# Kernel tuning notes

Hardware: AMD Instinct MI355X
Metric: run time of the kernel (lower is better)

## Reference

```python
import math
import jax, jax.numpy as jnp
from jax import lax
import numpy as np

B, S2, D = 8, 1024, 768  # seq_len = 32*32 spatial tokens
HD = 64                   # head_dim
K = 7                     # LocalRmsNorm kernel_size
EPS = 1e-7


def setup_inputs() -> dict:
    key = jax.random.key(0)
    ks = jax.random.split(key, 6)
    sc = 0.02
    return {
        "x": jax.random.normal(ks[0], (B, S2, D), jnp.float32),
        "norm_w": jnp.ones((D,), jnp.float32),
        "wq": jax.random.normal(ks[1], (D, D), jnp.float32) * sc,
        "bq": jnp.zeros((D,), jnp.float32),
        "wk": jax.random.normal(ks[2], (D, D), jnp.float32) * sc,
        "bk": jnp.zeros((D,), jnp.float32),
        "wv": jax.random.normal(ks[3], (D, D), jnp.float32) * sc,
        "bv": jnp.zeros((D,), jnp.float32),
        "wo": jax.random.normal(ks[4], (D, D), jnp.float32) * sc,
        "bo": jnp.zeros((D,), jnp.float32),
    }


def local_rms_norm(x, w):
    # x: [b, s*s, d]; sliding KxK box-sum of squares over the s x s grid,
    # zero-padded (matches F.unfold), mean divisor is always K*K.
    b, ss, d = x.shape
    s = int(math.isqrt(ss))
    sq = (x * x).reshape(b, s, s, d)
    box = lax.reduce_window(sq, 0.0, lax.add,
                            (1, K, K, 1), (1, 1, 1, 1), 'SAME')
    rms = jnp.sqrt(EPS + box / (K * K)).reshape(b, ss, d)
    return x / rms * w


def reference(x, norm_w, wq, bq, wk, bk, wv, bv, wo, bo):
    xn = local_rms_norm(x, norm_w)
    b, s, d = xn.shape
    h = d // HD

    def proj(w_, b_):
        return (xn @ w_.T + b_).reshape(b, s, h, HD).transpose(0, 2, 1, 3)

    q = proj(wq, bq)  # [b, h, s, dh]
    k = proj(wk, bk)
    v = proj(wv, bv)
    scores = jnp.einsum('bhqd,bhkd->bhqk', q, k) / math.sqrt(HD)
    attn = jax.nn.softmax(scores, axis=-1)
    out = jnp.einsum('bhqk,bhkd->bhqd', attn, v)
    out = out.transpose(0, 2, 1, 3).reshape(b, s, d)
    return out @ wo.T + bo
```

## Files before the change

### kernel.cpp

```cpp
#include <hip/hip_runtime.h>

typedef _Float16 f16x8 __attribute__((ext_vector_type(8)));
typedef _Float16 f16x4 __attribute__((ext_vector_type(4)));
typedef _Float16 f16x2 __attribute__((ext_vector_type(2)));
typedef float    f32x4 __attribute__((ext_vector_type(4)));
typedef float    f32x16 __attribute__((ext_vector_type(16)));
typedef unsigned int u32x4 __attribute__((ext_vector_type(4)));
typedef unsigned short ushort_t;
typedef unsigned int uint_t;

#define LOG2E 1.44269504088896340736f

__device__ __forceinline__ ushort_t f2h(float x) {
  _Float16 h = (_Float16)x;
  return __builtin_bit_cast(ushort_t, h);
}

__device__ __forceinline__ uint_t packpair(float a, float b) {
  return __builtin_bit_cast(uint_t, __builtin_amdgcn_cvt_pkrtz(a, b));
}

__device__ __forceinline__ f16x8 mk8(uint_t a, uint_t b, uint_t c, uint_t d) {
  u32x4 t; t[0] = a; t[1] = b; t[2] = c; t[3] = d;
  return __builtin_bit_cast(f16x8, t);
}

__device__ __forceinline__ void gload_lds16(const void* g, void* lds) {
  __builtin_amdgcn_global_load_lds(
      (const __attribute__((address_space(1))) void*)(uintptr_t)g,
      (__attribute__((address_space(3))) void*)(unsigned)(uintptr_t)lds,
      16, 0, 0);
}


__global__ __launch_bounds__(256)
void lrn_a(const float* __restrict__ x, ushort_t* __restrict__ tmp) {
  int tid = blockIdx.x * 256 + threadIdx.x;
  int dv  = tid % 192;
  int rem = tid / 192;
  int pos = rem & 1023;
  int b   = rem >> 10;
  int r = pos >> 5, c = pos & 31;
  const float4* base = (const float4*)x + ((size_t)b * 1024 + (size_t)r * 32) * 192 + dv;
  float ax = 0.f, ay = 0.f, az = 0.f, aw = 0.f;
#pragma unroll
  for (int dc = -3; dc <= 3; ++dc) {
    int cc = c + dc;
    if (cc >= 0 && cc < 32) {
      float4 v = base[cc * 192];
      ax += v.x * v.x; ay += v.y * v.y; az += v.z * v.z; aw += v.w * v.w;
    }
  }
  f16x4 o;
  o[0] = (_Float16)ax; o[1] = (_Float16)ay; o[2] = (_Float16)az; o[3] = (_Float16)aw;
  *(f16x4*)(tmp + (size_t)tid * 4) = o;
}

__global__ __launch_bounds__(256)
void lrn_b(const float* __restrict__ x, const ushort_t* __restrict__ tmp,
           const float* __restrict__ wn, ushort_t* __restrict__ xn) {
  int tid = blockIdx.x * 256 + threadIdx.x;
  int dv  = tid % 192;
  int rem = tid / 192;
  int pos = rem & 1023;
  int b   = rem >> 10;
  int r = pos >> 5, c = pos & 31;
  const ushort_t* tb = tmp + (((size_t)b * 1024 + c) * 192 + dv) * 4;
  float ax = 0.f, ay = 0.f, az = 0.f, aw = 0.f;
#pragma unroll
  for (int dr = -3; dr <= 3; ++dr) {
    int rr = r + dr;
    if (rr >= 0 && rr < 32) {
      f16x4 v = *(const f16x4*)(tb + (size_t)rr * 24576);
      ax += (float)v[0]; ay += (float)v[1]; az += (float)v[2]; aw += (float)v[3];
    }
  }
  float4 xv = ((const float4*)x)[tid];
  float4 wv = ((const float4*)wn)[dv];
  const float inv49 = 1.0f / 49.0f;
  float i0 = 1.0f / sqrtf(1e-7f + ax * inv49);
  float i1 = 1.0f / sqrtf(1e-7f + ay * inv49);
  float i2 = 1.0f / sqrtf(1e-7f + az * inv49);
  float i3 = 1.0f / sqrtf(1e-7f + aw * inv49);
  f16x4 o;
  o[0] = (_Float16)(xv.x * i0 * wv.x);
  o[1] = (_Float16)(xv.y * i1 * wv.y);
  o[2] = (_Float16)(xv.z * i2 * wv.z);
  o[3] = (_Float16)(xv.w * i3 * wv.w);
  const int m = b * 1024 + pos;
  const int panel = m >> 4, lrr = m & 15;
  const int kc = dv >> 3, lg2 = (dv >> 1) & 3, half = dv & 1;
  *(f16x4*)(xn + ((size_t)((panel * 24 + kc) * 64 + lg2 * 16 + lrr)) * 8 + half * 4) = o;
}

__global__ __launch_bounds__(256)
void convw_fm(const float* __restrict__ wq, const float* __restrict__ wk,
              const float* __restrict__ wv, const float* __restrict__ wo,
              ushort_t* __restrict__ bqkv, ushort_t* __restrict__ bwo) {
  const int g = blockIdx.x * 256 + threadIdx.x;
  const int mat = g / 73728;
  const int gg = g % 73728;
  const int panel = gg / 1536;
  const int rem = gg % 1536;
  const int kc = rem >> 6, l = rem & 63;
  const int row = panel * 16 + (l & 15);
  const int col = kc * 32 + (l >> 4) * 8;
  const float* src = (mat == 0) ? wq : (mat == 1) ? wk : (mat == 2) ? wv : wo;
  const float4 v0 = *(const float4*)(src + (size_t)row * 768 + col);
  const float4 v1 = *(const float4*)(src + (size_t)row * 768 + col + 4);
  f16x8 o;
  o[0]=(_Float16)v0.x; o[1]=(_Float16)v0.y; o[2]=(_Float16)v0.z; o[3]=(_Float16)v0.w;
  o[4]=(_Float16)v1.x; o[5]=(_Float16)v1.y; o[6]=(_Float16)v1.z; o[7]=(_Float16)v1.w;
  if (mat < 3) *(f16x8*)(bqkv + (size_t)g * 8) = o;
  else         *(f16x8*)(bwo  + (size_t)gg * 8) = o;
}

#define LOADSET(AS, BS, KT) do {                                                  \
    _Pragma("unroll")                                                             \
    for (int i = 0; i < 4; ++i) AS[i] = *(const f16x8*)(pa[i] + (KT) * 512);      \
    _Pragma("unroll")                                                             \
    for (int i = 0; i < 4; ++i) BS[i] = *(const f16x8*)(pb[i] + (KT) * 512);      \
  } while (0)

#define MFMASET(AS, BS) do {                                                      \
    _Pragma("unroll")                                                             \
    for (int mt = 0; mt < 4; ++mt)                                                \
      _Pragma("unroll")                                                           \
      for (int nt = 0; nt < 4; ++nt)                                              \
        acc[mt][nt] = __builtin_amdgcn_mfma_f32_16x16x32_f16(AS[mt], BS[nt], acc[mt][nt], 0, 0, 0); \
  } while (0)

template <int MODE>
__global__ __launch_bounds__(MODE == 0 ? 256 : 128)
void gemmfm(const ushort_t* __restrict__ Afm, const ushort_t* __restrict__ Bfm,
            const float* __restrict__ b0, const float* __restrict__ b1,
            const float* __restrict__ b2,
            ushort_t* __restrict__ q, ushort_t* __restrict__ k,
            ushort_t* __restrict__ v, float* __restrict__ outf) {
  const int bid = blockIdx.x;
  const int t = bid >> 3;
  const int bn = t >> 3;
  const int bm = (bid & 7) * 8 + (t & 7);
  const int tid = threadIdx.x;
  const int w = tid >> 6, l = tid & 63;
  const int lr = l & 15, lg = l >> 4;
  const int wr = (MODE == 0) ? (w >> 1) : w;
  const int wc = (MODE == 0) ? (w & 1) : 0;

  f32x4 acc[4][4] = {};

  const ushort_t* pa[4];
  const ushort_t* pb[4];
#pragma unroll
  for (int i = 0; i < 4; ++i) {
    pa[i] = Afm + ((size_t)((bm * 8 + wr * 4 + i) * 24) * 64 + l) * 8;
    pb[i] = Bfm + ((size_t)((bn * (MODE == 0 ? 8 : 4) + wc * 4 + i) * 24) * 64 + l) * 8;
  }

  f16x8 sA[4], sB[4], tA[4], tB[4];
  LOADSET(sA, sB, 0);
  for (int kt = 0; kt < 24; kt += 2) {
    LOADSET(tA, tB, kt + 1);
    MFMASET(sA, sB);
    if (kt + 2 < 24) LOADSET(sA, sB, kt + 2);
    MFMASET(tA, tB);
  }

#pragma unroll
  for (int mt = 0; mt < 4; ++mt) {
#pragma unroll
    for (int nt = 0; nt < 4; ++nt) {
      if (MODE == 0) {
        const int n = bn * 128 + wc * 64 + nt * 16 + lr;
        const int mbase = bm * 128 + wr * 64 + mt * 16 + lg * 4;
        const int region = n / 768;
        const int nn = n - region * 768;
        const int hh = nn >> 6, hd = nn & 63;
        const float bb = (region == 0 ? b0 : region == 1 ? b1 : b2)[nn];
        if (region == 2) {
          const int bi = mbase >> 10, s0 = mbase & 1023;
          const int tile = s0 >> 6, q6 = s0 & 63;
          const int aa = q6 >> 5, r5 = q6 & 31;
          const int t1 = r5 >> 3, h2 = (r5 >> 2) & 1;
          const int gq = t1 >> 1, jj = (2 * t1) & 3;
          const int s0p = (tile << 6) + (((aa << 1) + gq) << 4) + (h2 << 3) + 2 * jj;
          f16x4 pv;
#pragma unroll
          for (int gi = 0; gi < 4; ++gi) pv[gi] = (_Float16)(acc[mt][nt][gi] + bb);
          *(f16x4*)(v + (((size_t)(bi * 12 + hh)) * 64 + hd) * 1024 + s0p) = pv;
        } else {
#pragma unroll
          for (int gi = 0; gi < 4; ++gi) {
            const int m = mbase + gi;
            const int bi = m >> 10, s = m & 1023;
            const float val = acc[mt][nt][gi] + bb;
            if (region == 0)
              q[(((size_t)(bi * 12 + hh)) * 1024 + s) * 64 + hd] = f2h(val * (0.125f * LOG2E));
            else
              k[(((size_t)(bi * 12 + hh)) * 1024 + s) * 64 + hd] = f2h(val);
          }
        }
      } else {
        const int n = bn * 64 + nt * 16 + lr;
        const float bb = b0[n];
#pragma unroll
        for (int gi = 0; gi < 4; ++gi) {
          const int m = bm * 128 + w * 64 + mt * 16 + lg * 4 + gi;
          outf[(size_t)m * 768 + n] = acc[mt][nt][gi] + bb;
        }
      }
    }
  }
}

#define ATILE(T, CUR, NXT) do {                                                   \
    if ((T) < 15) {                                                               \
      const int kv0n = ((T) + 1) << 6;                                            \
      gload_lds16(kp + (size_t)(kv0n + r1) * 64 + s1 * 8,  Kl0 + (NXT) * 8192);   \
      gload_lds16(kp + (size_t)(kv0n + r2) * 64 + s2 * 8,  Kl1 + (NXT) * 8192);   \
      gload_lds16(vp + (size_t)r1 * 1024 + kv0n + s1 * 8,  Vl0 + (NXT) * 8192);   \
      gload_lds16(vp + (size_t)r2 * 1024 + kv0n + s2 * 8,  Vl1 + (NXT) * 8192);   \
    }                                                                             \
    const char* kbase = (const char*)smem + (CUR) * 8192;                         \
    const char* vbase = (const char*)smem + 16384 + (CUR) * 8192;                 \
    f16x8 ka0[4], ka1[4];                                                         \
    _Pragma("unroll")                                                             \
    for (int kc = 0; kc < 4; ++kc) {                                              \
      ka0[kc] = *(const f16x8*)(kbase + off[kc]);                                 \
      ka1[kc] = *(const f16x8*)(kbase + off[kc] + 4096);                          \
    }                                                                             \
    f32x16 s0v = {}, s1v = {};                                                    \
    __builtin_amdgcn_s_setprio(1);                                                \
    _Pragma("unroll")                                                             \
    for (int kc = 0; kc < 4; ++kc) {                                              \
      s0v = __builtin_amdgcn_mfma_f32_32x32x16_f16(ka0[kc], qf[kc], s0v, 0, 0, 0);\
      s1v = __builtin_amdgcn_mfma_f32_32x32x16_f16(ka1[kc], qf[kc], s1v, 0, 0, 0);\
    }                                                                             \
    __builtin_amdgcn_s_setprio(0);                                                \
    f16x8 va0[4], va1[4];                                                         \
    _Pragma("unroll")                                                             \
    for (int c = 0; c < 4; ++c) {                                                 \
      va0[c] = *(const f16x8*)(vbase + off[c]);                                   \
      va1[c] = *(const f16x8*)(vbase + off[c] + 4096);                            \
    }                                                                             \
    uint_t pk0[8], pk1[8];                                                        \
    _Pragma("unroll")                                                             \
    for (int tt = 0; tt < 8; ++tt) {                                              \
      pk0[tt] = packpair(__builtin_exp2f(s0v[2 * tt]), __builtin_exp2f(s0v[2 * tt + 1])); \
      pk1[tt] = packpair(__builtin_exp2f(s1v[2 * tt]), __builtin_exp2f(s1v[2 * tt + 1])); \
    }                                                                             \
    _Pragma("unroll")                                                             \
    for (int tt = 0; tt < 4; ++tt) {                                              \
      lr0 = __builtin_amdgcn_fdot2(__builtin_bit_cast(f16x2, pk0[tt]),     one2, lr0, false); \
      lr1 = __builtin_amdgcn_fdot2(__builtin_bit_cast(f16x2, pk0[tt + 4]), one2, lr1, false); \
      lr2 = __builtin_amdgcn_fdot2(__builtin_bit_cast(f16x2, pk1[tt]),     one2, lr2, false); \
      lr3 = __builtin_amdgcn_fdot2(__builtin_bit_cast(f16x2, pk1[tt + 4]), one2, lr3, false); \
    }                                                                             \
    const f16x8 pb0 = mk8(pk0[0], pk0[1], pk0[2], pk0[3]);                        \
    const f16x8 pb1 = mk8(pk0[4], pk0[5], pk0[6], pk0[7]);                        \
    const f16x8 pb2 = mk8(pk1[0], pk1[1], pk1[2], pk1[3]);                        \
    const f16x8 pb3 = mk8(pk1[4], pk1[5], pk1[6], pk1[7]);                        \
    __builtin_amdgcn_s_setprio(1);                                                \
    oacc0 = __builtin_amdgcn_mfma_f32_32x32x16_f16(va0[0], pb0, oacc0, 0, 0, 0);  \
    oacc1 = __builtin_amdgcn_mfma_f32_32x32x16_f16(va1[0], pb0, oacc1, 0, 0, 0);  \
    oacc0 = __builtin_amdgcn_mfma_f32_32x32x16_f16(va0[1], pb1, oacc0, 0, 0, 0);  \
    oacc1 = __builtin_amdgcn_mfma_f32_32x32x16_f16(va1[1], pb1, oacc1, 0, 0, 0);  \
    oacc0 = __builtin_amdgcn_mfma_f32_32x32x16_f16(va0[2], pb2, oacc0, 0, 0, 0);  \
    oacc1 = __builtin_amdgcn_mfma_f32_32x32x16_f16(va1[2], pb2, oacc1, 0, 0, 0);  \
    oacc0 = __builtin_amdgcn_mfma_f32_32x32x16_f16(va0[3], pb3, oacc0, 0, 0, 0);  \
    oacc1 = __builtin_amdgcn_mfma_f32_32x32x16_f16(va1[3], pb3, oacc1, 0, 0, 0);  \
    __builtin_amdgcn_s_setprio(0);                                                \
    __syncthreads();                                                              \
  } while (0)

__global__ __launch_bounds__(256, 3)
void attn_fused6(const ushort_t* __restrict__ qb, const ushort_t* __restrict__ kb,
                 const ushort_t* __restrict__ vt, ushort_t* __restrict__ ao) {
  __shared__ __align__(16) ushort_t smem[16384];
  const int tid = threadIdx.x;
  const int w = tid >> 6, l = tid & 63;
  const int lq = l & 31, hi = l >> 5;

  const int bid = blockIdx.x;
  const int cid = (bid & 7) * 96 + (bid >> 3);
  const int bh = cid >> 3, qt = cid & 7;
  const int b = bh / 12, h = bh % 12;

  const ushort_t* qp = qb + ((size_t)bh * 1024 + qt * 128 + w * 32) * 64;
  const ushort_t* kp = kb + (size_t)bh * 65536;
  const ushort_t* vp = vt + (size_t)bh * 65536;

  f16x8 qf[4];
#pragma unroll
  for (int kc = 0; kc < 4; ++kc)
    qf[kc] = *(const f16x8*)(qp + lq * 64 + kc * 16 + hi * 8);

  const int r1 = tid >> 3,          s1 = (tid & 7) ^ (r1 & 7);
  const int r2 = (tid + 256) >> 3,  s2 = (tid & 7) ^ (r2 & 7);
  char* Kl0 = (char*)smem + w * 1024;
  char* Kl1 = (char*)smem + 4096 + w * 1024;
  char* Vl0 = (char*)smem + 16384 + w * 1024;
  char* Vl1 = (char*)smem + 16384 + 4096 + w * 1024;

  const int cswz = lq & 7;
  int off[4];
#pragma unroll
  for (int kc = 0; kc < 4; ++kc)
    off[kc] = lq * 128 + (((kc * 2 + hi) ^ cswz) * 16);

  f32x16 oacc0 = {}, oacc1 = {};
  float lr0 = 0.f, lr1 = 0.f, lr2 = 0.f, lr3 = 0.f;
  const f16x2 one2 = {(_Float16)1.f, (_Float16)1.f};

  gload_lds16(kp + (size_t)r1 * 64 + s1 * 8,   Kl0);
  gload_lds16(kp + (size_t)r2 * 64 + s2 * 8,   Kl1);
  gload_lds16(vp + (size_t)r1 * 1024 + s1 * 8, Vl0);
  gload_lds16(vp + (size_t)r2 * 1024 + s2 * 8, Vl1);
  __syncthreads();

  for (int t2 = 0; t2 < 16; t2 += 2) {
    ATILE(t2, 0, 1);
    ATILE(t2 + 1, 1, 0);
  }

  float lrun = (lr0 + lr1) + (lr2 + lr3);
  lrun += __shfl_xor(lrun, 32, 64);
  const float invl = 1.0f / lrun;

  uint_t* ot = (uint_t*)smem + w * 1024 + lq * 32;
#pragma unroll
  for (int tt = 0; tt < 8; ++tt) {
    const int base = (tt & 1) + ((tt >> 1) << 2) + 2 * hi;
    ot[base ^ lq]        = packpair(oacc0[2 * tt] * invl, oacc0[2 * tt + 1] * invl);
    ot[(base + 16) ^ lq] = packpair(oacc1[2 * tt] * invl, oacc1[2 * tt + 1] * invl);
  }
  __syncthreads();
  const int row = tid >> 1, halfc = tid & 1;
  const int w2 = row >> 5, qq = row & 31;
  const uint_t* srcp = (const uint_t*)smem + w2 * 1024 + qq * 32;
  const int m = b * 1024 + qt * 128 + row;
  const int panel = m >> 4, lrr = m & 15;
  const int kc = h * 2 + halfc;
#pragma unroll
  for (int jj = 0; jj < 4; ++jj) {
    u32x4 tv;
#pragma unroll
    for (int i2 = 0; i2 < 4; ++i2)
      tv[i2] = srcp[(halfc * 16 + jj * 4 + i2) ^ qq];
    *(u32x4*)(ao + ((size_t)((panel * 24 + kc) * 64 + jj * 16 + lrr)) * 8) = tv;
  }
}

extern "C" void kernel_launch(void* const* d_in, const int* in_sizes, int n_in,
                              void* d_out, int out_size, void* d_ws, size_t ws_size,
                              hipStream_t stream) {
  const float* x  = (const float*)d_in[0];
  const float* nw = (const float*)d_in[1];
  const float* wq = (const float*)d_in[2];
  const float* bq = (const float*)d_in[3];
  const float* wk = (const float*)d_in[4];
  const float* bk = (const float*)d_in[5];
  const float* wv = (const float*)d_in[6];
  const float* bv = (const float*)d_in[7];
  const float* wo = (const float*)d_in[8];
  const float* bo = (const float*)d_in[9];
  float* out = (float*)d_out;

  char* ws = (char*)d_ws;
  ushort_t* tmp   = (ushort_t*)ws;
  ushort_t* qbuf  = (ushort_t*)(ws);
  ushort_t* kbuf  = (ushort_t*)(ws + 12582912);
  ushort_t* xnf   = (ushort_t*)(ws + 25165824);
  ushort_t* bwqkv = (ushort_t*)(ws + 37748736);
  ushort_t* bwo   = (ushort_t*)(ws + 41287680);
  ushort_t* vtb   = (ushort_t*)(ws + 42467328);
  ushort_t* aoutf = (ushort_t*)(ws + 55050240);

  lrn_a<<<6144, 256, 0, stream>>>(x, tmp);
  lrn_b<<<6144, 256, 0, stream>>>(x, tmp, nw, xnf);
  convw_fm<<<1152, 256, 0, stream>>>(wq, wk, wv, wo, bwqkv, bwo);
  gemmfm<0><<<1152, 256, 0, stream>>>(xnf, bwqkv, bq, bk, bv,
                                      qbuf, kbuf, vtb, nullptr);
  attn_fused6<<<768, 256, 0, stream>>>(qbuf, kbuf, vtb, aoutf);
  gemmfm<1><<<768, 128, 0, stream>>>(aoutf, bwo, bo, nullptr, nullptr,
                                     nullptr, nullptr, nullptr, out);
}
```

Measured before the change: 157.1 us.

## Stage GEMM tiles through LDS with async loads and split-barrier attention pipeline

Both projection GEMMs now stream A and B panels into double-buffered LDS using async global-to-LDS loads instead of having each wave load its fragments directly from global memory into registers. Sharing the panels across waves removes the redundant global reads that waves in the same row or column were each making. The output-projection GEMM is reshaped to 64x128 tiles with 256 threads. The attention loop replaces its trailing __syncthreads with explicit vmcnt waits plus a barrier at the start of each tile, so that the next tile's prefetch overlaps with compute. The hand-written waitcnt counts and barriers carry a risk of correctness bugs if the number of outstanding loads does not match the counts.

```diff
diff --git a/kernel.cpp b/kernel.cpp
--- a/kernel.cpp
+++ b/kernel.cpp
@@ -10,6 +10,12 @@
 typedef unsigned int uint_t;
 
 #define LOG2E 1.44269504088896340736f
+
+#define CFENCE  asm volatile("" ::: "memory")
+#define HWBAR   __builtin_amdgcn_s_barrier()
+#define VMCNT0  asm volatile("s_waitcnt vmcnt(0)" ::: "memory")
+#define VMCNT3  asm volatile("s_waitcnt vmcnt(3)" ::: "memory")
+#define VMCNT4  asm volatile("s_waitcnt vmcnt(4)" ::: "memory")
 
 __device__ __forceinline__ ushort_t f2h(float x) {
   _Float16 h = (_Float16)x;
@@ -115,61 +121,85 @@
   else         *(f16x8*)(bwo  + (size_t)gg * 8) = o;
 }
 
-#define LOADSET(AS, BS, KT) do {                                                  \
-    _Pragma("unroll")                                                             \
-    for (int i = 0; i < 4; ++i) AS[i] = *(const f16x8*)(pa[i] + (KT) * 512);      \
-    _Pragma("unroll")                                                             \
-    for (int i = 0; i < 4; ++i) BS[i] = *(const f16x8*)(pb[i] + (KT) * 512);      \
+#define GSTAGE(BUF, KT) do {                                                      \
+    _Pragma("unroll")                                                             \
+    for (int j = 0; j < SI; ++j)                                                  \
+      gload_lds16(sb[j] + (KT) * 512, (BUF) ? d1[j] : d0[j]);                     \
   } while (0)
 
-#define MFMASET(AS, BS) do {                                                      \
-    _Pragma("unroll")                                                             \
-    for (int mt = 0; mt < 4; ++mt)                                                \
+#define GTILE(KT, CUR, NXT) do {                                                  \
+    CFENCE; HWBAR; CFENCE;                              \
+    if ((KT) + 1 < 24) {                                                          \
+      GSTAGE(NXT, (KT) + 1);                                                      \
+      if constexpr (SI == 4) VMCNT4; else VMCNT3;       \
+    } else VMCNT0;                                                                \
+    CFENCE; HWBAR;                                \
+    __builtin_amdgcn_sched_barrier(0);                                            \
+    f16x8 af[MT], bf[NT];                                                         \
+    _Pragma("unroll")                                                             \
+    for (int mt = 0; mt < MT; ++mt)                                               \
+      af[mt] = *(const f16x8*)(&As[CUR][(wr * MT + mt) * 512 + l * 8]);           \
+    _Pragma("unroll")                                                             \
+    for (int nt = 0; nt < NT; ++nt)                                               \
+      bf[nt] = *(const f16x8*)(&Bs[CUR][(wc * NT + nt) * 512 + l * 8]);           \
+    _Pragma("unroll")                                                             \
+    for (int mt = 0; mt < MT; ++mt)                                               \
       _Pragma("unroll")                                                           \
-      for (int nt = 0; nt < 4; ++nt)                                              \
-        acc[mt][nt] = __builtin_amdgcn_mfma_f32_16x16x32_f16(AS[mt], BS[nt], acc[mt][nt], 0, 0, 0); \
+      for (int nt = 0; nt < NT; ++nt)                                             \
+        acc[mt][nt] = __builtin_amdgcn_mfma_f32_16x16x32_f16(af[mt], bf[nt], acc[mt][nt], 0, 0, 0); \
   } while (0)
 
 template <int MODE>
-__global__ __launch_bounds__(MODE == 0 ? 256 : 128)
-void gemmfm(const ushort_t* __restrict__ Afm, const ushort_t* __restrict__ Bfm,
-            const float* __restrict__ b0, const float* __restrict__ b1,
-            const float* __restrict__ b2,
-            ushort_t* __restrict__ q, ushort_t* __restrict__ k,
-            ushort_t* __restrict__ v, float* __restrict__ outf) {
+__global__ __launch_bounds__(256)
+void gemm_lds(const ushort_t* __restrict__ Afm, const ushort_t* __restrict__ Bfm,
+              const float* __restrict__ b0, const float* __restrict__ b1,
+              const float* __restrict__ b2,
+              ushort_t* __restrict__ q, ushort_t* __restrict__ k,
+              ushort_t* __restrict__ v, float* __restrict__ outf) {
+  constexpr int PM  = (MODE == 0) ? 8 : 4;
+  constexpr int PN  = 8;
+  constexpr int NBN = (MODE == 0) ? 18 : 6;
+  constexpr int SI  = (PM + PN) / 4;
+  constexpr int MT  = PM / 2, NT = PN / 2;
+  __shared__ __align__(16) ushort_t As[2][PM * 512];
+  __shared__ __align__(16) ushort_t Bs[2][PN * 512];
+
+  const int nwg = gridDim.x;
   const int bid = blockIdx.x;
-  const int t = bid >> 3;
-  const int bn = t >> 3;
-  const int bm = (bid & 7) * 8 + (t & 7);
+  const int cid = (bid & 7) * (nwg >> 3) + (bid >> 3);
+  const int bm = cid / NBN, bn = cid % NBN;
   const int tid = threadIdx.x;
   const int w = tid >> 6, l = tid & 63;
+  const int wr = w >> 1, wc = w & 1;
   const int lr = l & 15, lg = l >> 4;
-  const int wr = (MODE == 0) ? (w >> 1) : w;
-  const int wc = (MODE == 0) ? (w & 1) : 0;
-
-  f32x4 acc[4][4] = {};
-
-  const ushort_t* pa[4];
-  const ushort_t* pb[4];
-#pragma unroll
-  for (int i = 0; i < 4; ++i) {
-    pa[i] = Afm + ((size_t)((bm * 8 + wr * 4 + i) * 24) * 64 + l) * 8;
-    pb[i] = Bfm + ((size_t)((bn * (MODE == 0 ? 8 : 4) + wc * 4 + i) * 24) * 64 + l) * 8;
-  }
-
-  f16x8 sA[4], sB[4], tA[4], tB[4];
-  LOADSET(sA, sB, 0);
+
+  f32x4 acc[MT][NT] = {};
+
+  const ushort_t* sb[SI];
+  ushort_t* d0[SI];
+  ushort_t* d1[SI];
+#pragma unroll
+  for (int j = 0; j < SI; ++j) {
+    const int g = w * SI + j;
+    if (g < PM) {
+      sb[j] = Afm + ((size_t)(bm * PM + g) * 24) * 512 + l * 8;
+      d0[j] = &As[0][g * 512]; d1[j] = &As[1][g * 512];
+    } else {
+      sb[j] = Bfm + ((size_t)(bn * PN + (g - PM)) * 24) * 512 + l * 8;
+      d0[j] = &Bs[0][(g - PM) * 512]; d1[j] = &Bs[1][(g - PM) * 512];
+    }
+  }
+
+  GSTAGE(0, 0);
   for (int kt = 0; kt < 24; kt += 2) {
-    LOADSET(tA, tB, kt + 1);
-    MFMASET(sA, sB);
-    if (kt + 2 < 24) LOADSET(sA, sB, kt + 2);
-    MFMASET(tA, tB);
-  }
-
-#pragma unroll
-  for (int mt = 0; mt < 4; ++mt) {
-#pragma unroll
-    for (int nt = 0; nt < 4; ++nt) {
+    GTILE(kt, 0, 1);
+    GTILE(kt + 1, 1, 0);
+  }
+
+#pragma unroll
+  for (int mt = 0; mt < MT; ++mt) {
+#pragma unroll
+    for (int nt = 0; nt < NT; ++nt) {
       if (MODE == 0) {
         const int n = bn * 128 + wc * 64 + nt * 16 + lr;
         const int mbase = bm * 128 + wr * 64 + mt * 16 + lg * 4;
@@ -201,11 +231,11 @@
           }
         }
       } else {
-        const int n = bn * 64 + nt * 16 + lr;
+        const int n = bn * 128 + wc * 64 + nt * 16 + lr;
         const float bb = b0[n];
 #pragma unroll
         for (int gi = 0; gi < 4; ++gi) {
-          const int m = bm * 128 + w * 64 + mt * 16 + lg * 4 + gi;
+          const int m = bm * 64 + wr * 32 + mt * 16 + lg * 4 + gi;
           outf[(size_t)m * 768 + n] = acc[mt][nt][gi] + bb;
         }
       }
@@ -214,13 +244,17 @@
 }
 
 #define ATILE(T, CUR, NXT) do {                                                   \
+    CFENCE; HWBAR; CFENCE;                              \
     if ((T) < 15) {                                                               \
       const int kv0n = ((T) + 1) << 6;                                            \
       gload_lds16(kp + (size_t)(kv0n + r1) * 64 + s1 * 8,  Kl0 + (NXT) * 8192);   \
       gload_lds16(kp + (size_t)(kv0n + r2) * 64 + s2 * 8,  Kl1 + (NXT) * 8192);   \
       gload_lds16(vp + (size_t)r1 * 1024 + kv0n + s1 * 8,  Vl0 + (NXT) * 8192);   \
       gload_lds16(vp + (size_t)r2 * 1024 + kv0n + s2 * 8,  Vl1 + (NXT) * 8192);   \
-    }                                                                             \
+      VMCNT4;                                        \
+    } else VMCNT0;                                                                \
+    CFENCE; HWBAR;                            \
+    __builtin_amdgcn_sched_barrier(0);                                            \
     const char* kbase = (const char*)smem + (CUR) * 8192;                         \
     const char* vbase = (const char*)smem + 16384 + (CUR) * 8192;                 \
     f16x8 ka0[4], ka1[4];                                                         \
@@ -270,11 +304,10 @@
     oacc0 = __builtin_amdgcn_mfma_f32_32x32x16_f16(va0[3], pb3, oacc0, 0, 0, 0);  \
     oacc1 = __builtin_amdgcn_mfma_f32_32x32x16_f16(va1[3], pb3, oacc1, 0, 0, 0);  \
     __builtin_amdgcn_s_setprio(0);                                                \
-    __syncthreads();                                                              \
   } while (0)
 
 __global__ __launch_bounds__(256, 3)
-void attn_fused6(const ushort_t* __restrict__ qb, const ushort_t* __restrict__ kb,
+void attn_fused7(const ushort_t* __restrict__ qb, const ushort_t* __restrict__ kb,
                  const ushort_t* __restrict__ vt, ushort_t* __restrict__ ao) {
   __shared__ __align__(16) ushort_t smem[16384];
   const int tid = threadIdx.x;
@@ -316,7 +349,6 @@
   gload_lds16(kp + (size_t)r2 * 64 + s2 * 8,   Kl1);
   gload_lds16(vp + (size_t)r1 * 1024 + s1 * 8, Vl0);
   gload_lds16(vp + (size_t)r2 * 1024 + s2 * 8, Vl1);
-  __syncthreads();
 
   for (int t2 = 0; t2 < 16; t2 += 2) {
     ATILE(t2, 0, 1);
@@ -326,6 +358,8 @@
   float lrun = (lr0 + lr1) + (lr2 + lr3);
   lrun += __shfl_xor(lrun, 32, 64);
   const float invl = 1.0f / lrun;
+
+  __syncthreads();
 
   uint_t* ot = (uint_t*)smem + w * 1024 + lq * 32;
 #pragma unroll
@@ -379,9 +413,9 @@
   lrn_a<<<6144, 256, 0, stream>>>(x, tmp);
   lrn_b<<<6144, 256, 0, stream>>>(x, tmp, nw, xnf);
   convw_fm<<<1152, 256, 0, stream>>>(wq, wk, wv, wo, bwqkv, bwo);
-  gemmfm<0><<<1152, 256, 0, stream>>>(xnf, bwqkv, bq, bk, bv,
-                                      qbuf, kbuf, vtb, nullptr);
-  attn_fused6<<<768, 256, 0, stream>>>(qbuf, kbuf, vtb, aoutf);
-  gemmfm<1><<<768, 128, 0, stream>>>(aoutf, bwo, bo, nullptr, nullptr,
-                                     nullptr, nullptr, nullptr, out);
-}
+  gemm_lds<0><<<1152, 256, 0, stream>>>(xnf, bwqkv, bq, bk, bv,
+                                        qbuf, kbuf, vtb, nullptr);
+  attn_fused7<<<768, 256, 0, stream>>>(qbuf, kbuf, vtb, aoutf);
+  gemm_lds<1><<<768, 256, 0, stream>>>(aoutf, bwo, bo, nullptr, nullptr,
+                                       nullptr, nullptr, nullptr, out);
+}
```

Result: faster. 147.3 us (-6.2%).
